# Performance work log

Measured on AMD Instinct MI355X. Metric: run time of the kernel, lower is better.

The kernel has to match this reference:

```python
import jax, jax.numpy as jnp
import numpy as np

# ---- static config (matches init_kwargs) ----
B, N_CAMS, C, H, W = 2, 6, 256, 32, 88
BEV_H = BEV_W = 100
NQ = BEV_H * BEV_W
D_PILLAR = 4
HEADS = 8
LEVELS = 3
HEAD_DIM = C // HEADS
PC_RANGE = (-51.2, -51.2, -5.0, 51.2, 51.2, 3.0)
OGFH, OGFW = 256, 704


def _make_lidar2img():
    """Plausible lidar->image projection matrices (K @ [R|t]) for 6 ring cameras."""
    mats = np.zeros((B, N_CAMS, 4, 4), np.float32)
    K = np.array([[557.0, 0.0, OGFW / 2.0], [0.0, 557.0, OGFH / 2.0], [0.0, 0.0, 1.0]], np.float64)
    for b in range(B):
        for n in range(N_CAMS):
            yaw = 2.0 * np.pi * n / N_CAMS + 0.05 * b
            fwd = np.array([np.cos(yaw), np.sin(yaw), 0.0])
            right = np.array([np.sin(yaw), -np.cos(yaw), 0.0])
            down = np.array([0.0, 0.0, -1.0])
            R = np.stack([right, down, fwd])  # lidar -> camera axes
            cam_center = np.array([1.5 * np.cos(yaw), 1.5 * np.sin(yaw), 1.8])
            t = -R @ cam_center
            P = K @ np.concatenate([R, t[:, None]], axis=1)
            mats[b, n, :3, :] = P.astype(np.float32)
            mats[b, n, 3, 3] = 1.0
    return jnp.asarray(mats)


def setup_inputs() -> dict:
    key = jax.random.key(0)
    ks = jax.random.split(key, 16)
    s = 0.02
    return {
        'imgs': jax.random.normal(ks[0], (B, N_CAMS, C, H, W), jnp.float32),
        'lidar2img': _make_lidar2img(),
        'bev_query': jax.random.normal(ks[1], (NQ, 1, C), jnp.float32) * s,
        'bev_pos': jax.random.normal(ks[2], (1, NQ, C), jnp.float32) * s,
        'cams_embeds': jax.random.normal(ks[3], (N_CAMS, C), jnp.float32) * s,
        'level_embeds': jax.random.normal(ks[4], (LEVELS, C), jnp.float32) * s,
        'w_fpn': jax.random.normal(ks[5], (LEVELS, C, C), jnp.float32) * s,
        'b_fpn': jnp.zeros((LEVELS, C), jnp.float32),
        'w_value': jax.random.normal(ks[6], (C, C), jnp.float32) * s,
        'b_value': jnp.zeros((C,), jnp.float32),
        'w_off': jax.random.normal(ks[7], (C, HEADS * LEVELS * D_PILLAR * 2), jnp.float32) * s,
        'b_off': jax.random.normal(ks[8], (HEADS * LEVELS * D_PILLAR * 2,), jnp.float32) * 0.5,
        'w_attn': jax.random.normal(ks[9], (C, HEADS * LEVELS * D_PILLAR), jnp.float32) * s,
        'b_attn': jnp.zeros((HEADS * LEVELS * D_PILLAR,), jnp.float32),
        'w_out': jax.random.normal(ks[10], (C, C), jnp.float32) * s,
        'b_out': jnp.zeros((C,), jnp.float32),
        'w_ts1': jax.random.normal(ks[11], (C, C), jnp.float32) * s,
        'b_ts1': jnp.zeros((C,), jnp.float32),
        'w_ts2': jax.random.normal(ks[12], (C, C), jnp.float32) * s,
        'b_ts2': jnp.zeros((C,), jnp.float32),
    }


def _deform_sample(v, loc, h, w):
    """Bilinear sample (grid_sample, zero padding, align_corners=False).
    v: [N, heads, h*w, dh]; loc: [N, heads, Q, 2] normalized to [0,1]. -> [N, heads, Q, dh]"""
    x = loc[..., 0] * w - 0.5
    y = loc[..., 1] * h - 0.5
    x0 = jnp.floor(x)
    y0 = jnp.floor(y)
    out = jnp.zeros(v.shape[:2] + (loc.shape[2], v.shape[-1]), v.dtype)
    for dx in (0, 1):
        for dy in (0, 1):
            xi = x0 + dx
            yi = y0 + dy
            wgt = (1.0 - jnp.abs(x - xi)) * (1.0 - jnp.abs(y - yi))
            valid = (xi >= 0) & (xi < w) & (yi >= 0) & (yi < h)
            idx = (jnp.clip(yi, 0, h - 1) * w + jnp.clip(xi, 0, w - 1)).astype(jnp.int32)
            g = jnp.take_along_axis(v, idx[..., None], axis=2)
            out = out + g * (wgt * valid)[..., None]
    return out


def _forward(imgs, lidar2img, bev_query, bev_pos, cams_embeds, level_embeds,
             w_fpn, b_fpn, w_value, b_value, w_off, b_off, w_attn, b_attn,
             w_out, b_out, w_ts1, b_ts1, w_ts2, b_ts2):
    # ---- FPN: 3 levels at strides 1/2/4 with per-level 1x1 projection ----
    x = imgs.reshape(B * N_CAMS, C, H, W)
    feats, shapes = [], []
    cur = x
    for l in range(LEVELS):
        if l > 0:
            bn, c, h, w = cur.shape
            cur = cur.reshape(bn, c, h // 2, 2, w // 2, 2).mean(axis=(3, 5))
        f = jnp.einsum('bchw,cd->bdhw', cur, w_fpn[l]) + b_fpn[l][None, :, None, None]
        feats.append(f)
        shapes.append((f.shape[2], f.shape[3]))
    # ---- flatten levels + cam/level embeds: [N, sum_hw, B, C] ----
    flat = []
    for l, f in enumerate(feats):
        h, w = shapes[l]
        fl = jnp.transpose(f.reshape(B, N_CAMS, C, h * w), (1, 0, 3, 2))  # [N,B,hw,C]
        fl = fl + cams_embeds[:, None, None, :] + level_embeds[l][None, None, None, :]
        flat.append(fl)
    feat_flatten = jnp.transpose(jnp.concatenate(flat, axis=2), (0, 2, 1, 3))  # [N,sum_hw,B,C]

    # ---- 3D pillar reference points, normalized [0,1] ----
    zrange = PC_RANGE[5] - PC_RANGE[2]
    zs = jnp.linspace(0.5, zrange - 0.5, D_PILLAR) / zrange
    xs = (jnp.arange(BEV_W, dtype=jnp.float32) + 0.5) / BEV_W
    ys = (jnp.arange(BEV_H, dtype=jnp.float32) + 0.5) / BEV_H
    gy, gx = jnp.meshgrid(ys, xs, indexing='ij')
    ref2d = jnp.stack([gx.ravel(), gy.ravel()], axis=-1)  # [NQ,2]
    ref3d = jnp.concatenate([
        jnp.broadcast_to(ref2d[None], (D_PILLAR, NQ, 2)),
        jnp.broadcast_to(zs[:, None, None].astype(jnp.float32), (D_PILLAR, NQ, 1)),
    ], axis=-1)
    scale = jnp.array([PC_RANGE[3] - PC_RANGE[0], PC_RANGE[4] - PC_RANGE[1], zrange], jnp.float32)
    shift = jnp.array(PC_RANGE[:3], jnp.float32)
    xyz = ref3d * scale + shift
    homog = jnp.concatenate([xyz, jnp.ones((D_PILLAR, NQ, 1), jnp.float32)], axis=-1)

    # ---- point sampling: project to each camera, mask invalid pixels ----
    pts = jnp.einsum('bnij,dqj->nbqdi', lidar2img, homog)  # [N,B,NQ,D,4]
    eps = 1e-5
    depth = pts[..., 2]
    xy = pts[..., :2] / jnp.maximum(depth[..., None], eps)
    ref_cam = xy / jnp.array([OGFW, OGFH], jnp.float32)  # [N,B,NQ,D,2]
    bev_mask = ((depth > eps) & (ref_cam[..., 0] > 0) & (ref_cam[..., 0] < 1)
                & (ref_cam[..., 1] > 0) & (ref_cam[..., 1] < 1))  # [N,B,NQ,D]

    pos = bev_pos[0]  # [NQ,C]

    def sca(query, value, ref_b, mask_b):
        # query [NQ,C]; value [N,sum_hw,C]; ref_b [N,NQ,D,2]; mask_b [N,NQ,D]
        residual = query
        q = query + pos
        v = value @ w_value + b_value
        off = (q @ w_off + b_off).reshape(NQ, HEADS, LEVELS, D_PILLAR, 2)
        attn = jax.nn.softmax((q @ w_attn + b_attn).reshape(NQ, HEADS, LEVELS * D_PILLAR), axis=-1)
        attn = attn.reshape(NQ, HEADS, LEVELS, D_PILLAR)
        out = jnp.zeros((N_CAMS, NQ, HEADS, HEAD_DIM), q.dtype)
        start = 0
        for l, (h, w) in enumerate(shapes):
            hw = h * w
            v_l = jnp.transpose(v[:, start:start + hw].reshape(N_CAMS, hw, HEADS, HEAD_DIM), (0, 2, 1, 3))
            start += hw
            norm = jnp.array([w, h], q.dtype)
            loc = ref_b[:, :, None, :, :] + off[None, :, :, l] / norm  # [N,NQ,heads,D,2]
            loc = jnp.transpose(loc, (0, 2, 1, 3, 4)).reshape(N_CAMS, HEADS, NQ * D_PILLAR, 2)
            s = _deform_sample(v_l, loc, h, w).reshape(N_CAMS, HEADS, NQ, D_PILLAR, HEAD_DIM)
            out = out + jnp.einsum('nhqpd,qhp->nqhd', s, attn[:, :, l])
        out = out.reshape(N_CAMS, NQ, C)
        valid = mask_b.any(axis=-1)  # [N,NQ]
        slots = (out * valid[..., None].astype(out.dtype)).sum(axis=0)
        count = jnp.maximum(valid.sum(axis=0), 1).astype(out.dtype)[:, None]
        slots = slots / count
        return slots @ w_out + b_out + residual

    def tsblock(t):
        return jax.nn.relu(t @ w_ts1 + b_ts1) @ w_ts2 + b_ts2

    bq = jnp.transpose(bev_query, (1, 0, 2))[0]  # [NQ,C]
    groups = []
    ego = bq
    for b in range(B):
        val = feat_flatten[:, :, b, :]
        r = ref_cam[:, b]
        m = bev_mask[:, b]
        if b == 0:
            for _ in range(2):
                bq = tsblock(sca(bq, val, r, m))
            ego = bq
            groups.append(ego.reshape(C, BEV_W, BEV_H))
        else:
            nb = tsblock(sca(ego, val, r, m))
            groups.append(nb.reshape(C, BEV_W, BEV_H))
    bev_groups = jnp.stack(groups, axis=0)  # [B,C,BEV_W,BEV_H]
    return bq[None], bev_groups


def reference(imgs, lidar2img, bev_query, bev_pos, cams_embeds, level_embeds,
              w_fpn, b_fpn, w_value, b_value, w_off, b_off, w_attn, b_attn,
              w_out, b_out, w_ts1, b_ts1, w_ts2, b_ts2):
    return _forward(imgs, lidar2img, bev_query, bev_pos, cams_embeds, level_embeds,
                    w_fpn, b_fpn, w_value, b_value, w_off, b_off, w_attn, b_attn,
                    w_out, b_out, w_ts1, b_ts1, w_ts2, b_ts2)
```

## Files before the change

kernel.cpp:

```cpp
#include <hip/hip_runtime.h>
#include <math.h>

typedef __attribute__((ext_vector_type(8))) short bf16x8;
typedef __attribute__((ext_vector_type(4))) float f32x4;

__device__ __forceinline__ unsigned short f2bf(float x) {
  union { float f; unsigned int u; } v; v.f = x;
  unsigned int r = v.u + 0x7fffu + ((v.u >> 16) & 1u);
  return (unsigned short)(r >> 16);
}
__device__ __forceinline__ float bf2f(unsigned short b) {
  union { unsigned int u; float f; } v; v.u = ((unsigned int)b) << 16; return v.f;
}
__device__ __forceinline__ void split2(float x, unsigned short& h, unsigned short& l) {
  h = f2bf(x);
  l = f2bf(x - bf2f(h));
}
__device__ __forceinline__ int fsi(int q, int c) { return q * 256 + (c ^ ((q & 7) << 2)); }

__device__ __forceinline__ void ld16(const unsigned short* b, bf16x8* f) {
  const unsigned short* b1 = b + 2048;
  const unsigned short* b2 = b + 4096;
  const unsigned short* b3 = b + 6144;
  asm volatile(
    "global_load_dwordx4 %0, %16, off\n\t"
    "global_load_dwordx4 %1, %16, off offset:1024\n\t"
    "global_load_dwordx4 %2, %16, off offset:2048\n\t"
    "global_load_dwordx4 %3, %16, off offset:3072\n\t"
    "global_load_dwordx4 %4, %17, off\n\t"
    "global_load_dwordx4 %5, %17, off offset:1024\n\t"
    "global_load_dwordx4 %6, %17, off offset:2048\n\t"
    "global_load_dwordx4 %7, %17, off offset:3072\n\t"
    "global_load_dwordx4 %8, %18, off\n\t"
    "global_load_dwordx4 %9, %18, off offset:1024\n\t"
    "global_load_dwordx4 %10, %18, off offset:2048\n\t"
    "global_load_dwordx4 %11, %18, off offset:3072\n\t"
    "global_load_dwordx4 %12, %19, off\n\t"
    "global_load_dwordx4 %13, %19, off offset:1024\n\t"
    "global_load_dwordx4 %14, %19, off offset:2048\n\t"
    "global_load_dwordx4 %15, %19, off offset:3072\n\t"
    "s_waitcnt vmcnt(0)"
    : "=&v"(f[0]), "=&v"(f[1]), "=&v"(f[2]), "=&v"(f[3]),
      "=&v"(f[4]), "=&v"(f[5]), "=&v"(f[6]), "=&v"(f[7]),
      "=&v"(f[8]), "=&v"(f[9]), "=&v"(f[10]), "=&v"(f[11]),
      "=&v"(f[12]), "=&v"(f[13]), "=&v"(f[14]), "=&v"(f[15])
    : "v"(b), "v"(b1), "v"(b2), "v"(b3));
}

#define MFMA(a, b, c) __builtin_amdgcn_mfma_f32_16x16x32_bf16(a, b, c, 0, 0, 0)

__device__ __forceinline__ void gemm2t32(
    const unsigned short* __restrict__ Wp, int tile0,
    int lane, int lk, int l15,
    const unsigned short (&AS)[2][32][32][8], f32x4 (&acc)[2][2])
{
  const unsigned short* base = Wp + ((size_t)(tile0 >> 1) * 16384) + (size_t)lane * 8;
  bf16x8 f[32];
  ld16(base, f);
  ld16(base + 8192, f + 16);
#pragma unroll
  for (int ks = 0; ks < 8; ++ks) {
    bf16x8 h0 = f[2 * ks], l0 = f[2 * ks + 1];
    bf16x8 h1 = f[16 + 2 * ks], l1 = f[17 + 2 * ks];
#pragma unroll
    for (int nf = 0; nf < 2; ++nf) {
      bf16x8 bqh = *(const bf16x8*)&AS[0][ks * 4 + lk][nf * 16 + l15][0];
      bf16x8 bql = *(const bf16x8*)&AS[1][ks * 4 + lk][nf * 16 + l15][0];
      acc[0][nf] = MFMA(h0, bqh, acc[0][nf]);
      acc[0][nf] = MFMA(h0, bql, acc[0][nf]);
      acc[0][nf] = MFMA(l0, bqh, acc[0][nf]);
      acc[1][nf] = MFMA(h1, bqh, acc[1][nf]);
      acc[1][nf] = MFMA(h1, bql, acc[1][nf]);
      acc[1][nf] = MFMA(l1, bqh, acc[1][nf]);
    }
  }
}

__device__ __forceinline__ void gemm2t64(
    const unsigned short* __restrict__ Wp, int tile0,
    int lane, int lk, int l15,
    const unsigned short (&AS)[2][32][64][8], f32x4 (&acc)[2][4])
{
  const unsigned short* base = Wp + ((size_t)(tile0 >> 1) * 16384) + (size_t)lane * 8;
  bf16x8 f[32];
  ld16(base, f);
  ld16(base + 8192, f + 16);
#pragma unroll
  for (int ks = 0; ks < 8; ++ks) {
    bf16x8 h0 = f[2 * ks], l0 = f[2 * ks + 1];
    bf16x8 h1 = f[16 + 2 * ks], l1 = f[17 + 2 * ks];
#pragma unroll
    for (int nf = 0; nf < 4; ++nf) {
      bf16x8 bqh = *(const bf16x8*)&AS[0][ks * 4 + lk][nf * 16 + l15][0];
      bf16x8 bql = *(const bf16x8*)&AS[1][ks * 4 + lk][nf * 16 + l15][0];
      acc[0][nf] = MFMA(h0, bqh, acc[0][nf]);
      acc[0][nf] = MFMA(h0, bql, acc[0][nf]);
      acc[0][nf] = MFMA(l0, bqh, acc[0][nf]);
      acc[1][nf] = MFMA(h1, bqh, acc[1][nf]);
      acc[1][nf] = MFMA(h1, bql, acc[1][nf]);
      acc[1][nf] = MFMA(l1, bqh, acc[1][nf]);
    }
  }
}

__device__ __forceinline__ void gemm1t64(
    const unsigned short* __restrict__ Wp, int tile,
    int lane, int lk, int l15,
    const unsigned short (&AS)[2][32][64][8], f32x4 (&acc)[4])
{
  const unsigned short* base = Wp + ((size_t)(tile >> 1) * 16384) + (size_t)(tile & 1) * 8192 + (size_t)lane * 8;
  bf16x8 f[16];
  ld16(base, f);
#pragma unroll
  for (int ks = 0; ks < 8; ++ks) {
    bf16x8 eh = f[2 * ks], el = f[2 * ks + 1];
#pragma unroll
    for (int nf = 0; nf < 4; ++nf) {
      bf16x8 bqh = *(const bf16x8*)&AS[0][ks * 4 + lk][nf * 16 + l15][0];
      bf16x8 bql = *(const bf16x8*)&AS[1][ks * 4 + lk][nf * 16 + l15][0];
      acc[nf] = MFMA(eh, bqh, acc[nf]);
      acc[nf] = MFMA(eh, bql, acc[nf]);
      acc[nf] = MFMA(el, bqh, acc[nf]);
    }
  }
}

__global__ __launch_bounds__(256) void pool2x2(const float* __restrict__ in, float* __restrict__ out,
                                               int h, int w, int total)
{
  int i = blockIdx.x * 256 + threadIdx.x;
  if (i >= total) return;
  int x = i % w; int r = i / w; int y = r % h; int ci = r / h;
  const float* p = in + (size_t)ci * (4 * h * w) + (size_t)(2 * y) * (2 * w) + 2 * x;
  out[i] = (p[0] + p[1] + p[2 * w] + p[2 * w + 1]) * 0.25f;
}

__global__ __launch_bounds__(256) void prep(
    const float* __restrict__ wo, const float* __restrict__ bo,
    const float* __restrict__ wa, const float* __restrict__ ba,
    const float* __restrict__ wout, const float* __restrict__ wts1, const float* __restrict__ wts2,
    const float* __restrict__ wfpn, const float* __restrict__ wval,
    const float* __restrict__ cams, const float* __restrict__ lev,
    const float* __restrict__ bfpn, const float* __restrict__ bval,
    unsigned short* __restrict__ wcatH, unsigned short* __restrict__ wcatL, float* __restrict__ bcat,
    unsigned short* __restrict__ woutH, unsigned short* __restrict__ woutL,
    unsigned short* __restrict__ wts1H, unsigned short* __restrict__ wts1L,
    unsigned short* __restrict__ w45H, unsigned short* __restrict__ w45L,
    unsigned short* __restrict__ wcombH, unsigned short* __restrict__ wcombL,
    float* __restrict__ e2)
{
  int bb = blockIdx.x, t = threadIdx.x;
  if (bb < 768) {
    int l = bb >> 8, i = bb & 255, j = t;
    const float* a = wfpn + ((size_t)l * 256 + i) * 256;
    float acc = 0.f;
    for (int k = 0; k < 256; ++k) acc = fmaf(a[k], wval[(size_t)k * 256 + j], acc);
    unsigned short h, lo; split2(acc, h, lo);
    size_t o = ((size_t)l * 256 + j) * 256 + i;
    wcombH[o] = h; wcombL[o] = lo;
  } else if (bb < 1056) {
    int i = (bb - 768) * 256 + t;
    int c = i >> 8, k = i & 255;
    float v = (c < 192) ? wo[k * 192 + c] : wa[k * 96 + (c - 192)];
    unsigned short h, l; split2(v, h, l);
    wcatH[i] = h; wcatL[i] = l;
    if (i < 288) bcat[i] = (i < 192) ? bo[i] : ba[i - 192];
  } else if (bb < 1312) {
    int i = (bb - 1056) * 256 + t;
    int nn = i >> 8, k = i & 255;
    float v = wout[(size_t)k * 256 + nn];
    unsigned short h, l; split2(v, h, l);
    woutH[i] = h; woutL[i] = l;
  } else if (bb < 1568) {
    int i = (bb - 1312) * 256 + t;
    int nn = i >> 8, k = i & 255;
    float v = wts1[(size_t)k * 256 + nn];
    unsigned short h, l; split2(v, h, l);
    wts1H[i] = h; wts1L[i] = l;
  } else if (bb < 1824) {
    int i = (bb - 1568) * 256 + t;
    int nn = i >> 8, k = i & 255;
    float v = wts2[(size_t)k * 256 + nn];
    unsigned short h, l; split2(v, h, l);
    w45H[i] = h; w45L[i] = l;
  } else if (bb < 2112) {
    int mp = bb - 1824;
    int k = t;
    float acc = 0.f;
    for (int j = 0; j < 256; ++j) {
      float wc = (mp < 192) ? wo[j * 192 + mp] : wa[j * 96 + (mp - 192)];
      acc = fmaf(wts2[(size_t)k * 256 + j], wc, acc);
    }
    unsigned short h, l; split2(acc, h, l);
    size_t o = (size_t)(256 + mp) * 256 + k;
    w45H[o] = h; w45L[o] = l;
  } else {
    int e = bb - 2112;
    int n = e / 3, l = e % 3, j = t;
    float acc = bval[j];
    for (int k = 0; k < 256; ++k) {
      float s = cams[n * 256 + k] + lev[l * 256 + k] + bfpn[l * 256 + k];
      acc = fmaf(s, wval[(size_t)k * 256 + j], acc);
    }
    e2[(size_t)e * 256 + j] = acc;
  }
}

__global__ __launch_bounds__(256) void relayout(
    const unsigned short* __restrict__ wcombH, const unsigned short* __restrict__ wcombL,
    const unsigned short* __restrict__ wcatH, const unsigned short* __restrict__ wcatL,
    const unsigned short* __restrict__ woutH, const unsigned short* __restrict__ woutL,
    const unsigned short* __restrict__ wts1H, const unsigned short* __restrict__ wts1L,
    const unsigned short* __restrict__ w45H, const unsigned short* __restrict__ w45L,
    unsigned short* __restrict__ wcombP, unsigned short* __restrict__ wcatP,
    unsigned short* __restrict__ woutP, unsigned short* __restrict__ wts1P,
    unsigned short* __restrict__ w45P)
{
  int bb = blockIdx.x, t = threadIdx.x;
  const unsigned short *H, *L; unsigned short* P; int tile;
  if (bb < 48)      { H = wcombH; L = wcombL; P = wcombP; tile = bb; }
  else if (bb < 66) { H = wcatH;  L = wcatL;  P = wcatP;  tile = bb - 48; }
  else if (bb < 82) { H = woutH;  L = woutL;  P = woutP;  tile = bb - 66; }
  else if (bb < 98) { H = wts1H;  L = wts1L;  P = wts1P;  tile = bb - 82; }
  else              { H = w45H;   L = w45L;   P = w45P;   tile = bb - 98; }
#pragma unroll
  for (int e = 0; e < 32; ++e) {
    int idx = t * 32 + e;
    int slot = idx >> 9;
    int lane = (idx >> 3) & 63;
    int j8 = idx & 7;
    int ks = slot >> 1, hl = slot & 1;
    int col = tile * 16 + (lane & 15);
    int k = ks * 32 + (lane >> 4) * 8 + j8;
    size_t dst = ((size_t)(tile >> 1) * 16384) + (size_t)(((tile & 1) << 4) + slot) * 512 + (size_t)lane * 8 + j8;
    P[dst] = (hl ? L : H)[(size_t)col * 256 + k];
  }
}

__global__ __launch_bounds__(512) void value_fused(
    const float* __restrict__ img0, const float* __restrict__ cur1, const float* __restrict__ cur2,
    const unsigned short* __restrict__ wcombP,
    const float* __restrict__ e2, float* __restrict__ V)
{
  __shared__ __align__(16) unsigned short AS[2][32][32][8];
  int t = threadIdx.x, wid = t >> 6, lane = t & 63, l15 = lane & 15, lk = lane >> 4;
  int bx = blockIdx.x, cam = blockIdx.y;
  int level, tb, hw; const float* src;
  if (bx < 88)       { level = 0; tb = bx;       hw = 2816; src = img0; }
  else if (bx < 110) { level = 1; tb = bx - 88;  hw = 704;  src = cur1; }
  else               { level = 2; tb = bx - 110; hw = 176;  src = cur2; }
  int p0 = tb * 32;
  const int LST[3] = {0, 2816, 3520};
  src += (size_t)cam * 256 * hw;

  {
    int f4g = t & 7, kb = t >> 3;
    bool full = (p0 + 32 <= hw);
#pragma unroll
    for (int j = 0; j < 4; ++j) {
      int k = kb + j * 64;
      const float* row = src + (size_t)k * hw;
      int p = p0 + 4 * f4g;
      float4 v;
      if (full) v = *(const float4*)(row + p);
      else {
        v.x = (p < hw) ? row[p] : 0.f;     v.y = (p + 1 < hw) ? row[p + 1] : 0.f;
        v.z = (p + 2 < hw) ? row[p + 2] : 0.f; v.w = (p + 3 < hw) ? row[p + 3] : 0.f;
      }
      int ch = k >> 3, ko = k & 7;
      unsigned short h, l;
      split2(v.x, h, l); AS[0][ch][4 * f4g + 0][ko] = h; AS[1][ch][4 * f4g + 0][ko] = l;
      split2(v.y, h, l); AS[0][ch][4 * f4g + 1][ko] = h; AS[1][ch][4 * f4g + 1][ko] = l;
      split2(v.z, h, l); AS[0][ch][4 * f4g + 2][ko] = h; AS[1][ch][4 * f4g + 2][ko] = l;
      split2(v.w, h, l); AS[0][ch][4 * f4g + 3][ko] = h; AS[1][ch][4 * f4g + 3][ko] = l;
    }
  }
  __syncthreads();

  f32x4 zed = {0.f, 0.f, 0.f, 0.f};
  f32x4 acc[2][2] = {{zed, zed}, {zed, zed}};
  gemm2t32(wcombP, level * 16 + wid * 2, lane, lk, l15, AS, acc);
  __syncthreads();

  float* ASf = (float*)(&AS[0][0][0][0]);
  const float* bias = e2 + (size_t)(cam * 3 + level) * 256;
#pragma unroll
  for (int mf = 0; mf < 2; ++mf) {
    int chb = (wid * 2 + mf) * 16 + lk * 4;
    float4 b4 = *(const float4*)(bias + chb);
#pragma unroll
    for (int nf = 0; nf < 2; ++nf) {
      int q = nf * 16 + l15;
      float4 o;
      o.x = acc[mf][nf][0] + b4.x; o.y = acc[mf][nf][1] + b4.y;
      o.z = acc[mf][nf][2] + b4.z; o.w = acc[mf][nf][3] + b4.w;
      *(float4*)&ASf[fsi(q, chb)] = o;
    }
  }
  __syncthreads();
  float* Vb = V + ((size_t)cam * 3696 + LST[level] + p0) * 256;
#pragma unroll
  for (int j = 0; j < 4; ++j) {
    int g = t + j * 512;
    int q = g >> 6, c = (g & 63) * 4;
    if (p0 + q < hw)
      *(float4*)(Vb + (size_t)q * 256 + c) = *(const float4*)&ASf[fsi(q, c)];
  }
}

__global__ __launch_bounds__(512) void fused_iter(
    const float* __restrict__ slots, const float* __restrict__ qin,
    const float* __restrict__ pos2, const float* __restrict__ rowbias,
    const unsigned short* __restrict__ woutP, const unsigned short* __restrict__ wts1P,
    const unsigned short* __restrict__ w45P, const unsigned short* __restrict__ wcatP,
    const float* __restrict__ bout, const float* __restrict__ bts1,
    const float* __restrict__ bts2, const float* __restrict__ bcat,
    float* __restrict__ qout, float* __restrict__ outA, float* __restrict__ outB,
    float* __restrict__ qtmpA, float* __restrict__ qtmpB, int init)
{
  __shared__ __align__(16) unsigned short AS[2][32][64][8];
  float* ASf = (float*)(&AS[0][0][0][0]);
  int t = threadIdx.x, wid = t >> 6, lane = t & 63, l15 = lane & 15, lk = lane >> 4;
  int r0 = blockIdx.x * 64;
  f32x4 zed = {0.f, 0.f, 0.f, 0.f};

  {
    const float* base = init ? qin : slots;
#pragma unroll
    for (int j = 0; j < 8; ++j) {
      int g = t + j * 512;
      int q = g >> 6, c = (g & 63) * 4;
      int rq = r0 + q; if (rq > 9999) rq = 9999;
      float4 a = *(const float4*)(base + (size_t)rq * 256 + c);
      if (init) {
        if (pos2) {
          float4 p = *(const float4*)(pos2 + (size_t)rq * 256 + c);
          a.x += p.x; a.y += p.y; a.z += p.z; a.w += p.w;
        }
        if (rowbias) {
          float4 rb = *(const float4*)(rowbias + c);
          a.x += rb.x; a.y += rb.y; a.z += rb.z; a.w += rb.w;
        }
      }
      ushort4 hh, ll;
      split2(a.x, hh.x, ll.x); split2(a.y, hh.y, ll.y);
      split2(a.z, hh.z, ll.z); split2(a.w, hh.w, ll.w);
      *(ushort4*)&AS[0][c >> 3][q][c & 7] = hh;
      *(ushort4*)&AS[1][c >> 3][q][c & 7] = ll;
    }
  }
  __syncthreads();

  if (init) {
    f32x4 acc[2][4] = {{zed, zed, zed, zed}, {zed, zed, zed, zed}};
    gemm2t64(wcatP, wid * 2, lane, lk, l15, AS, acc);
    f32x4 acc3[4] = {zed, zed, zed, zed};
    if (wid < 2) gemm1t64(wcatP, 16 + wid, lane, lk, l15, AS, acc3);
    __syncthreads();
#pragma unroll
    for (int mf = 0; mf < 2; ++mf) {
      int chb = (wid * 2 + mf) * 16 + lk * 4;
      float4 b4 = *(const float4*)(bcat + chb);
#pragma unroll
      for (int nf = 0; nf < 4; ++nf) {
        int q = nf * 16 + l15;
        float4 o;
        o.x = acc[mf][nf][0] + b4.x; o.y = acc[mf][nf][1] + b4.y;
        o.z = acc[mf][nf][2] + b4.z; o.w = acc[mf][nf][3] + b4.w;
        *(float4*)&ASf[fsi(q, chb)] = o;
      }
    }
    if (wid < 2) {
      int ce = wid * 16 + lk * 4;
      float4 b4 = *(const float4*)(bcat + 256 + ce);
#pragma unroll
      for (int nf = 0; nf < 4; ++nf) {
        int qg = r0 + nf * 16 + l15;
        if (qg < 10000) {
          float4 o;
          o.x = acc3[nf][0] + b4.x; o.y = acc3[nf][1] + b4.y;
          o.z = acc3[nf][2] + b4.z; o.w = acc3[nf][3] + b4.w;
          *(float4*)(qtmpB + (size_t)qg * 32 + ce) = o;
        }
      }
    }
    __syncthreads();
#pragma unroll
    for (int j = 0; j < 8; ++j) {
      int g = t + j * 512;
      int q = g >> 6, c = (g & 63) * 4;
      int qg = r0 + q;
      if (qg < 10000)
        *(float4*)(qtmpA + (size_t)qg * 256 + c) = *(const float4*)&ASf[fsi(q, c)];
    }
    return;
  }

  {
    f32x4 acc[2][4] = {{zed, zed, zed, zed}, {zed, zed, zed, zed}};
    gemm2t64(woutP, wid * 2, lane, lk, l15, AS, acc);
    __syncthreads();
    float4 qreg[8];
#pragma unroll
    for (int j = 0; j < 8; ++j) {
      int g = t + j * 512;
      int q = g >> 6, c = (g & 63) * 4;
      int rq = r0 + q; if (rq > 9999) rq = 9999;
      qreg[j] = *(const float4*)(qin + (size_t)rq * 256 + c);
    }
#pragma unroll
    for (int j = 0; j < 8; ++j) {
      int g = t + j * 512;
      int q = g >> 6, c = (g & 63) * 4;
      *(float4*)&ASf[fsi(q, c)] = qreg[j];
    }
    __syncthreads();
    float4 rr[2][4];
#pragma unroll
    for (int mf = 0; mf < 2; ++mf) {
      int chb = (wid * 2 + mf) * 16 + lk * 4;
#pragma unroll
      for (int nf = 0; nf < 4; ++nf)
        rr[mf][nf] = *(const float4*)&ASf[fsi(nf * 16 + l15, chb)];
    }
    __syncthreads();
#pragma unroll
    for (int mf = 0; mf < 2; ++mf) {
      int chb = (wid * 2 + mf) * 16 + lk * 4;
      float4 b4 = *(const float4*)(bout + chb);
#pragma unroll
      for (int nf = 0; nf < 4; ++nf) {
        int q = nf * 16 + l15;
        float v0 = acc[mf][nf][0] + b4.x + rr[mf][nf].x;
        float v1 = acc[mf][nf][1] + b4.y + rr[mf][nf].y;
        float v2 = acc[mf][nf][2] + b4.z + rr[mf][nf].z;
        float v3 = acc[mf][nf][3] + b4.w + rr[mf][nf].w;
        ushort4 hh, ll;
        split2(v0, hh.x, ll.x); split2(v1, hh.y, ll.y);
        split2(v2, hh.z, ll.z); split2(v3, hh.w, ll.w);
        *(ushort4*)&AS[0][chb >> 3][q][chb & 7] = hh;
        *(ushort4*)&AS[1][chb >> 3][q][chb & 7] = ll;
      }
    }
    __syncthreads();
  }
  {
    f32x4 acc[2][4] = {{zed, zed, zed, zed}, {zed, zed, zed, zed}};
    gemm2t64(wts1P, wid * 2, lane, lk, l15, AS, acc);
    __syncthreads();
#pragma unroll
    for (int mf = 0; mf < 2; ++mf) {
      int chb = (wid * 2 + mf) * 16 + lk * 4;
      float4 b4 = *(const float4*)(bts1 + chb);
#pragma unroll
      for (int nf = 0; nf < 4; ++nf) {
        int q = nf * 16 + l15;
        float v0 = fmaxf(acc[mf][nf][0] + b4.x, 0.f);
        float v1 = fmaxf(acc[mf][nf][1] + b4.y, 0.f);
        float v2 = fmaxf(acc[mf][nf][2] + b4.z, 0.f);
        float v3 = fmaxf(acc[mf][nf][3] + b4.w, 0.f);
        ushort4 hh, ll;
        split2(v0, hh.x, ll.x); split2(v1, hh.y, ll.y);
        split2(v2, hh.z, ll.z); split2(v3, hh.w, ll.w);
        *(ushort4*)&AS[0][chb >> 3][q][chb & 7] = hh;
        *(ushort4*)&AS[1][chb >> 3][q][chb & 7] = ll;
      }
    }
    __syncthreads();
  }
  {
    f32x4 accA[2][4] = {{zed, zed, zed, zed}, {zed, zed, zed, zed}};
    f32x4 accB[2][4] = {{zed, zed, zed, zed}, {zed, zed, zed, zed}};
    if (wid < 4 || qtmpA) {
      gemm2t64(w45P, wid * 4,     lane, lk, l15, AS, accA);
      gemm2t64(w45P, wid * 4 + 2, lane, lk, l15, AS, accB);
    }
    f32x4 acc3[4] = {zed, zed, zed, zed};
    if (qtmpA && wid < 2) gemm1t64(w45P, 32 + wid, lane, lk, l15, AS, acc3);
    __syncthreads();
    if (wid < 4) {
#pragma unroll
      for (int half = 0; half < 2; ++half) {
#pragma unroll
        for (int mf = 0; mf < 2; ++mf) {
          int chb = (wid * 4 + half * 2 + mf) * 16 + lk * 4;
          float4 b4 = *(const float4*)(bts2 + chb);
#pragma unroll
          for (int nf = 0; nf < 4; ++nf) {
            int q = nf * 16 + l15;
            f32x4 a = half ? accB[mf][nf] : accA[mf][nf];
            float4 o;
            o.x = a[0] + b4.x; o.y = a[1] + b4.y;
            o.z = a[2] + b4.z; o.w = a[3] + b4.w;
            *(float4*)&ASf[fsi(q, chb)] = o;
          }
        }
      }
    }
    if (qtmpA && wid < 2) {
      int ce = wid * 16 + lk * 4;
#pragma unroll
      for (int nf = 0; nf < 4; ++nf) {
        int qg = r0 + nf * 16 + l15;
        if (qg < 10000) {
          float4 o;
          o.x = acc3[nf][0]; o.y = acc3[nf][1]; o.z = acc3[nf][2]; o.w = acc3[nf][3];
          *(float4*)(qtmpB + (size_t)qg * 32 + ce) = o;
        }
      }
    }
    __syncthreads();
#pragma unroll
    for (int j = 0; j < 8; ++j) {
      int g = t + j * 512;
      int q = g >> 6, c = (g & 63) * 4;
      int qg = r0 + q;
      if (qg < 10000) {
        float4 vq = *(const float4*)&ASf[fsi(q, c)];
        size_t go = (size_t)qg * 256 + c;
        *(float4*)(qout + go) = vq;
        if (outA) { *(float4*)(outA + go) = vq; *(float4*)(outB + go) = vq; }
      }
    }
    if (!qtmpA) return;
    __syncthreads();
    if (wid >= 4) {
#pragma unroll
      for (int half = 0; half < 2; ++half) {
#pragma unroll
        for (int mf = 0; mf < 2; ++mf) {
          int cc = ((wid - 4) * 4 + half * 2 + mf) * 16 + lk * 4;
#pragma unroll
          for (int nf = 0; nf < 4; ++nf) {
            int q = nf * 16 + l15;
            f32x4 a = half ? accB[mf][nf] : accA[mf][nf];
            float4 o;
            o.x = a[0]; o.y = a[1]; o.z = a[2]; o.w = a[3];
            *(float4*)&ASf[fsi(q, cc)] = o;
          }
        }
      }
    }
    __syncthreads();
#pragma unroll
    for (int j = 0; j < 8; ++j) {
      int g = t + j * 512;
      int q = g >> 6, c = (g & 63) * 4;
      int qg = r0 + q;
      if (qg < 10000)
        *(float4*)(qtmpA + (size_t)qg * 256 + c) = *(const float4*)&ASf[fsi(q, c)];
    }
  }
}

__global__ __launch_bounds__(256) void sca_sample(const float* __restrict__ qtmpA, const float* __restrict__ qtmpB,
                                                  const float* __restrict__ posA, const float* __restrict__ posB,
                                                  const float* __restrict__ V,
                                                  const float* __restrict__ l2i, float* __restrict__ slots)
{
  int b = blockIdx.x;
  int q = (b & 7) * 1250 + (b >> 3);
  int t = threadIdx.x;
  int head = t >> 5;
  __shared__ float raw[288];
  __shared__ float attnS[96];
  __shared__ float refx[6][4], refy[6][4];
  __shared__ int mnd[24];
  __shared__ int validn[6];
  __shared__ __align__(16) float w4[576][4];
  __shared__ __align__(16) int o4[576][4];

  {
    float x = qtmpA[(size_t)q * 256 + t];
    if (posA) x += posA[(size_t)q * 256 + t];
    raw[t] = x;
    if (t < 32) {
      float y = qtmpB[(size_t)q * 32 + t];
      if (posB) y += posB[(size_t)q * 32 + t];
      raw[256 + t] = y;
    }
  }
  if (t >= 32 && t < 56) {
    int tt = t - 32;
    int n = tt >> 2, d = tt & 3;
    const float* Mrow = l2i + n * 16;
    int qx = q % 100, qy = q / 100;
    float X = ((qx + 0.5f) / 100.0f) * 102.4f + (-51.2f);
    float Y = ((qy + 0.5f) / 100.0f) * 102.4f + (-51.2f);
    float zi = (d == 3) ? 7.5f : (0.5f + (float)d * (7.0f / 3.0f));
    float Z = zi + (-5.0f);
    float px = Mrow[0] * X + Mrow[1] * Y + Mrow[2] * Z + Mrow[3];
    float py = Mrow[4] * X + Mrow[5] * Y + Mrow[6] * Z + Mrow[7];
    float pz = Mrow[8] * X + Mrow[9] * Y + Mrow[10] * Z + Mrow[11];
    float dz = fmaxf(pz, 1e-5f);
    float xc = (px / dz) / 704.0f;
    float yc = (py / dz) / 256.0f;
    refx[n][d] = xc; refy[n][d] = yc;
    mnd[n * 4 + d] = (pz > 1e-5f) && (xc > 0.f) && (xc < 1.f) && (yc > 0.f) && (yc < 1.f);
  }
  __syncthreads();
  if (t < 8) {
    float mx = raw[192 + t * 12];
    for (int p = 1; p < 12; ++p) mx = fmaxf(mx, raw[192 + t * 12 + p]);
    float s = 0.f;
    float e[12];
#pragma unroll
    for (int p = 0; p < 12; ++p) { e[p] = __expf(raw[192 + t * 12 + p] - mx); s += e[p]; }
    float inv = 1.f / s;
#pragma unroll
    for (int p = 0; p < 12; ++p) attnS[t * 12 + p] = e[p] * inv;
  } else if (t < 14) {
    int n = t - 8;
    validn[n] = mnd[n * 4] | mnd[n * 4 + 1] | mnd[n * 4 + 2] | mnd[n * 4 + 3];
  }
  __syncthreads();

  int nv = validn[0] + validn[1] + validn[2] + validn[3] + validn[4] + validn[5];
  float invc = 1.f / (float)(nv > 1 ? nv : 1);

  const float WWf[3] = {88.f, 44.f, 22.f}, HHf[3] = {32.f, 16.f, 8.f};
  const int WWi[3] = {88, 44, 22}, STi[3] = {0, 2816, 3520};
  for (int pt = t; pt < 576; pt += 256) {
    int hd = pt & 7;
    int g = pt >> 3;
    int j = g % 12, n = g / 12;
    int l = j >> 2, d = j & 3;
    float wwf = WWf[l], hhf = HHf[l];
    int wwi = WWi[l], st = STi[l];
    float a = attnS[hd * 12 + j] * invc;
    float ox = raw[hd * 24 + l * 8 + d * 2 + 0];
    float oy = raw[hd * 24 + l * 8 + d * 2 + 1];
    float x = refx[n][d] * wwf + ox - 0.5f;
    float y = refy[n][d] * hhf + oy - 0.5f;
    float x0 = floorf(x), y0 = floorf(y);
    float fx = x - x0, fy = y - y0;
    float wx0 = 1.f - fx, wy0 = 1.f - fy;
    float vx0 = (x0 >= 0.f && x0 < wwf) ? 1.f : 0.f;
    float vx1 = (x0 + 1.f >= 0.f && x0 + 1.f < wwf) ? 1.f : 0.f;
    float vy0 = (y0 >= 0.f && y0 < hhf) ? 1.f : 0.f;
    float vy1 = (y0 + 1.f >= 0.f && y0 + 1.f < hhf) ? 1.f : 0.f;
    w4[pt][0] = a * wx0 * wy0 * vx0 * vy0;
    w4[pt][1] = a * fx * wy0 * vx1 * vy0;
    w4[pt][2] = a * wx0 * fy * vx0 * vy1;
    w4[pt][3] = a * fx * fy * vx1 * vy1;
    int ix0 = (int)fminf(fmaxf(x0, 0.f), wwf - 1.f);
    int ix1 = (int)fminf(fmaxf(x0 + 1.f, 0.f), wwf - 1.f);
    int iy0 = (int)fminf(fmaxf(y0, 0.f), hhf - 1.f);
    int iy1 = (int)fminf(fmaxf(y0 + 1.f, 0.f), hhf - 1.f);
    int rA = (st + iy0 * wwi) * 256, rB = (st + iy1 * wwi) * 256;
    o4[pt][0] = rA + ix0 * 256;
    o4[pt][1] = rA + ix1 * 256;
    o4[pt][2] = rB + ix0 * 256;
    o4[pt][3] = rB + ix1 * 256;
  }
  __syncthreads();

  float acc0 = 0.f, acc1 = 0.f;
#pragma unroll
  for (int n = 0; n < 6; ++n) {
    if (!validn[n]) continue;
    const float* Vn = V + (size_t)n * 946176 + t;
    int pb = n * 96 + head;
    float va[48];
#pragma unroll
    for (int j = 0; j < 12; ++j) {
      int4 o = *reinterpret_cast<const int4*>(&o4[pb + j * 8][0]);
      va[4 * j + 0] = Vn[o.x];
      va[4 * j + 1] = Vn[o.y];
      va[4 * j + 2] = Vn[o.z];
      va[4 * j + 3] = Vn[o.w];
    }
#pragma unroll
    for (int j = 0; j < 12; ++j) {
      float4 w = *reinterpret_cast<const float4*>(&w4[pb + j * 8][0]);
      acc0 = fmaf(w.x, va[4 * j + 0], acc0);
      acc1 = fmaf(w.y, va[4 * j + 1], acc1);
      acc0 = fmaf(w.z, va[4 * j + 2], acc0);
      acc1 = fmaf(w.w, va[4 * j + 3], acc1);
    }
  }
  slots[(size_t)q * 256 + t] = acc0 + acc1;
}

extern "C" void kernel_launch(void* const* d_in, const int* in_sizes, int n_in,
                              void* d_out, int out_size, void* d_ws, size_t ws_size,
                              hipStream_t stream)
{
  const float* imgs = (const float*)d_in[0];
  const float* l2i = (const float*)d_in[1];
  const float* bev_query = (const float*)d_in[2];
  const float* bev_pos = (const float*)d_in[3];
  const float* cams = (const float*)d_in[4];
  const float* lev = (const float*)d_in[5];
  const float* wfpn = (const float*)d_in[6];
  const float* bfpn = (const float*)d_in[7];
  const float* wval = (const float*)d_in[8];
  const float* bval = (const float*)d_in[9];
  const float* woff = (const float*)d_in[10];
  const float* boff = (const float*)d_in[11];
  const float* wattn = (const float*)d_in[12];
  const float* battn = (const float*)d_in[13];
  const float* wout = (const float*)d_in[14];
  const float* bout = (const float*)d_in[15];
  const float* wts1 = (const float*)d_in[16];
  const float* bts1 = (const float*)d_in[17];
  const float* wts2 = (const float*)d_in[18];
  const float* bts2 = (const float*)d_in[19];

  float* W = (float*)d_ws;
  size_t off = 0;
  auto alloc = [&](size_t n) { float* p = W + off; off += n; return p; };
  float* v    = alloc((size_t)6 * 3696 * 256);
  float* cur1 = alloc((size_t)12 * 256 * 16 * 44);
  float* cur2 = alloc((size_t)12 * 256 * 8 * 22);
  float* bqA  = alloc(2560000);
  float* bqB  = alloc(2560000);
  float* qtmpA = alloc(2560000);
  float* qtmpB = alloc(320000);
  float* posA = alloc(2560000);
  float* posB = alloc(320000);
  float* slots = alloc(2560000);
  float* wcatR = alloc(73728);
  float* woutR = alloc(65536);
  float* wts1R = alloc(65536);
  float* w45R = alloc(139264);
  float* wcombR = alloc(196608);
  float* wcombPR = alloc(196608);
  float* wcatPR = alloc(73728);
  float* woutPR = alloc(65536);
  float* wts1PR = alloc(65536);
  float* w45PR = alloc(139264);
  float* bcat = alloc(512);
  float* e2 = alloc(4608);
  (void)ws_size; (void)in_sizes; (void)n_in; (void)out_size;

  unsigned short* wcat_h = (unsigned short*)wcatR;   unsigned short* wcat_l = wcat_h + 288 * 256;
  unsigned short* wout_h = (unsigned short*)woutR;   unsigned short* wout_l = wout_h + 65536;
  unsigned short* wts1_h = (unsigned short*)wts1R;   unsigned short* wts1_l = wts1_h + 65536;
  unsigned short* w45_h = (unsigned short*)w45R;     unsigned short* w45_l = w45_h + 544 * 256;
  unsigned short* wcomb_h = (unsigned short*)wcombR; unsigned short* wcomb_l = wcomb_h + 3 * 65536;
  unsigned short* wcombP = (unsigned short*)wcombPR;
  unsigned short* wcatP = (unsigned short*)wcatPR;
  unsigned short* woutP = (unsigned short*)woutPR;
  unsigned short* wts1P = (unsigned short*)wts1PR;
  unsigned short* w45P = (unsigned short*)w45PR;

  float* OUT = (float*)d_out;

  pool2x2<<<8448, 256, 0, stream>>>(imgs, cur1, 16, 44, 2162688);
  pool2x2<<<2112, 256, 0, stream>>>(cur1, cur2, 8, 22, 540672);
  prep<<<2130, 256, 0, stream>>>(woff, boff, wattn, battn, wout, wts1, wts2, wfpn, wval,
                                 cams, lev, bfpn, bval,
                                 wcat_h, wcat_l, bcat, wout_h, wout_l, wts1_h, wts1_l,
                                 w45_h, w45_l, wcomb_h, wcomb_l, e2);
  relayout<<<132, 256, 0, stream>>>(wcomb_h, wcomb_l, wcat_h, wcat_l, wout_h, wout_l,
                                    wts1_h, wts1_l, w45_h, w45_l,
                                    wcombP, wcatP, woutP, wts1P, w45P);

  fused_iter<<<157, 512, 0, stream>>>(nullptr, bev_pos, nullptr, bts2,
      woutP, wts1P, w45P, wcatP, bout, bts1, bts2, bcat,
      nullptr, nullptr, nullptr, posA, posB, 1);
  fused_iter<<<157, 512, 0, stream>>>(nullptr, bev_query, bev_pos, nullptr,
      woutP, wts1P, w45P, wcatP, bout, bts1, bts2, bcat,
      nullptr, nullptr, nullptr, qtmpA, qtmpB, 1);

  value_fused<<<dim3(116, 6), 512, 0, stream>>>(imgs, cur1, cur2, wcombP, e2, v);

  sca_sample<<<10000, 256, 0, stream>>>(qtmpA, qtmpB, nullptr, nullptr, v, l2i, slots);
  fused_iter<<<157, 512, 0, stream>>>(slots, bev_query, nullptr, nullptr,
      woutP, wts1P, w45P, wcatP, bout, bts1, bts2, bcat,
      bqA, nullptr, nullptr, qtmpA, qtmpB, 0);
  sca_sample<<<10000, 256, 0, stream>>>(qtmpA, qtmpB, posA, posB, v, l2i, slots);
  fused_iter<<<157, 512, 0, stream>>>(slots, bqA, nullptr, nullptr,
      woutP, wts1P, w45P, wcatP, bout, bts1, bts2, bcat,
      bqB, OUT, OUT + 2560000, qtmpA, qtmpB, 0);

  value_fused<<<dim3(116, 6), 512, 0, stream>>>(imgs + (size_t)4325376, cur1 + (size_t)1081344,
                                                cur2 + (size_t)270336, wcombP, e2, v);
  sca_sample<<<10000, 256, 0, stream>>>(qtmpA, qtmpB, posA, posB, v, l2i + 96, slots);
  fused_iter<<<157, 512, 0, stream>>>(slots, bqB, nullptr, nullptr,
      woutP, wts1P, w45P, wcatP, bout, bts1, bts2, bcat,
      OUT + 5120000, nullptr, nullptr, nullptr, nullptr, 0);
}
```

Before: 320.7 us.

## Halve fused_iter row tile to 32 and compact valid-camera sampling points

```diff
diff --git a/kernel.cpp b/kernel.cpp
--- a/kernel.cpp
+++ b/kernel.cpp
@@ -76,37 +76,10 @@
   }
 }
 
-__device__ __forceinline__ void gemm2t64(
-    const unsigned short* __restrict__ Wp, int tile0,
-    int lane, int lk, int l15,
-    const unsigned short (&AS)[2][32][64][8], f32x4 (&acc)[2][4])
-{
-  const unsigned short* base = Wp + ((size_t)(tile0 >> 1) * 16384) + (size_t)lane * 8;
-  bf16x8 f[32];
-  ld16(base, f);
-  ld16(base + 8192, f + 16);
-#pragma unroll
-  for (int ks = 0; ks < 8; ++ks) {
-    bf16x8 h0 = f[2 * ks], l0 = f[2 * ks + 1];
-    bf16x8 h1 = f[16 + 2 * ks], l1 = f[17 + 2 * ks];
-#pragma unroll
-    for (int nf = 0; nf < 4; ++nf) {
-      bf16x8 bqh = *(const bf16x8*)&AS[0][ks * 4 + lk][nf * 16 + l15][0];
-      bf16x8 bql = *(const bf16x8*)&AS[1][ks * 4 + lk][nf * 16 + l15][0];
-      acc[0][nf] = MFMA(h0, bqh, acc[0][nf]);
-      acc[0][nf] = MFMA(h0, bql, acc[0][nf]);
-      acc[0][nf] = MFMA(l0, bqh, acc[0][nf]);
-      acc[1][nf] = MFMA(h1, bqh, acc[1][nf]);
-      acc[1][nf] = MFMA(h1, bql, acc[1][nf]);
-      acc[1][nf] = MFMA(l1, bqh, acc[1][nf]);
-    }
-  }
-}
-
-__device__ __forceinline__ void gemm1t64(
+__device__ __forceinline__ void gemm1t32(
     const unsigned short* __restrict__ Wp, int tile,
     int lane, int lk, int l15,
-    const unsigned short (&AS)[2][32][64][8], f32x4 (&acc)[4])
+    const unsigned short (&AS)[2][32][32][8], f32x4 (&acc)[2])
 {
   const unsigned short* base = Wp + ((size_t)(tile >> 1) * 16384) + (size_t)(tile & 1) * 8192 + (size_t)lane * 8;
   bf16x8 f[16];
@@ -115,7 +88,7 @@
   for (int ks = 0; ks < 8; ++ks) {
     bf16x8 eh = f[2 * ks], el = f[2 * ks + 1];
 #pragma unroll
-    for (int nf = 0; nf < 4; ++nf) {
+    for (int nf = 0; nf < 2; ++nf) {
       bf16x8 bqh = *(const bf16x8*)&AS[0][ks * 4 + lk][nf * 16 + l15][0];
       bf16x8 bql = *(const bf16x8*)&AS[1][ks * 4 + lk][nf * 16 + l15][0];
       acc[nf] = MFMA(eh, bqh, acc[nf]);
@@ -237,7 +210,7 @@
   }
 }
 
-__global__ __launch_bounds__(512) void value_fused(
+__global__ __launch_bounds__(512, 4) void value_fused(
     const float* __restrict__ img0, const float* __restrict__ cur1, const float* __restrict__ cur2,
     const unsigned short* __restrict__ wcombP,
     const float* __restrict__ e2, float* __restrict__ V)
@@ -308,7 +281,7 @@
   }
 }
 
-__global__ __launch_bounds__(512) void fused_iter(
+__global__ __launch_bounds__(512, 4) void fused_iter(
     const float* __restrict__ slots, const float* __restrict__ qin,
     const float* __restrict__ pos2, const float* __restrict__ rowbias,
     const unsigned short* __restrict__ woutP, const unsigned short* __restrict__ wts1P,
@@ -318,16 +291,16 @@
     float* __restrict__ qout, float* __restrict__ outA, float* __restrict__ outB,
     float* __restrict__ qtmpA, float* __restrict__ qtmpB, int init)
 {
-  __shared__ __align__(16) unsigned short AS[2][32][64][8];
+  __shared__ __align__(16) unsigned short AS[2][32][32][8];
   float* ASf = (float*)(&AS[0][0][0][0]);
   int t = threadIdx.x, wid = t >> 6, lane = t & 63, l15 = lane & 15, lk = lane >> 4;
-  int r0 = blockIdx.x * 64;
+  int r0 = blockIdx.x * 32;
   f32x4 zed = {0.f, 0.f, 0.f, 0.f};
 
   {
     const float* base = init ? qin : slots;
 #pragma unroll
-    for (int j = 0; j < 8; ++j) {
+    for (int j = 0; j < 4; ++j) {
       int g = t + j * 512;
       int q = g >> 6, c = (g & 63) * 4;
       int rq = r0 + q; if (rq > 9999) rq = 9999;
@@ -352,17 +325,17 @@
   __syncthreads();
 
   if (init) {
-    f32x4 acc[2][4] = {{zed, zed, zed, zed}, {zed, zed, zed, zed}};
-    gemm2t64(wcatP, wid * 2, lane, lk, l15, AS, acc);
-    f32x4 acc3[4] = {zed, zed, zed, zed};
-    if (wid < 2) gemm1t64(wcatP, 16 + wid, lane, lk, l15, AS, acc3);
+    f32x4 acc[2][2] = {{zed, zed}, {zed, zed}};
+    gemm2t32(wcatP, wid * 2, lane, lk, l15, AS, acc);
+    f32x4 acc3[2] = {zed, zed};
+    if (wid < 2) gemm1t32(wcatP, 16 + wid, lane, lk, l15, AS, acc3);
     __syncthreads();
 #pragma unroll
     for (int mf = 0; mf < 2; ++mf) {
       int chb = (wid * 2 + mf) * 16 + lk * 4;
       float4 b4 = *(const float4*)(bcat + chb);
 #pragma unroll
-      for (int nf = 0; nf < 4; ++nf) {
+      for (int nf = 0; nf < 2; ++nf) {
         int q = nf * 16 + l15;
         float4 o;
         o.x = acc[mf][nf][0] + b4.x; o.y = acc[mf][nf][1] + b4.y;
@@ -374,7 +347,7 @@
       int ce = wid * 16 + lk * 4;
       float4 b4 = *(const float4*)(bcat + 256 + ce);
 #pragma unroll
-      for (int nf = 0; nf < 4; ++nf) {
+      for (int nf = 0; nf < 2; ++nf) {
         int qg = r0 + nf * 16 + l15;
         if (qg < 10000) {
           float4 o;
@@ -386,7 +359,7 @@
     }
     __syncthreads();
 #pragma unroll
-    for (int j = 0; j < 8; ++j) {
+    for (int j = 0; j < 4; ++j) {
       int g = t + j * 512;
       int q = g >> 6, c = (g & 63) * 4;
       int qg = r0 + q;
@@ -397,30 +370,30 @@
   }
 
   {
-    f32x4 acc[2][4] = {{zed, zed, zed, zed}, {zed, zed, zed, zed}};
-    gemm2t64(woutP, wid * 2, lane, lk, l15, AS, acc);
-    __syncthreads();
-    float4 qreg[8];
-#pragma unroll
-    for (int j = 0; j < 8; ++j) {
+    f32x4 acc[2][2] = {{zed, zed}, {zed, zed}};
+    gemm2t32(woutP, wid * 2, lane, lk, l15, AS, acc);
+    __syncthreads();
+    float4 qreg[4];
+#pragma unroll
+    for (int j = 0; j < 4; ++j) {
       int g = t + j * 512;
       int q = g >> 6, c = (g & 63) * 4;
       int rq = r0 + q; if (rq > 9999) rq = 9999;
       qreg[j] = *(const float4*)(qin + (size_t)rq * 256 + c);
     }
 #pragma unroll
-    for (int j = 0; j < 8; ++j) {
+    for (int j = 0; j < 4; ++j) {
       int g = t + j * 512;
       int q = g >> 6, c = (g & 63) * 4;
       *(float4*)&ASf[fsi(q, c)] = qreg[j];
     }
     __syncthreads();
-    float4 rr[2][4];
+    float4 rr[2][2];
 #pragma unroll
     for (int mf = 0; mf < 2; ++mf) {
       int chb = (wid * 2 + mf) * 16 + lk * 4;
 #pragma unroll
-      for (int nf = 0; nf < 4; ++nf)
+      for (int nf = 0; nf < 2; ++nf)
         rr[mf][nf] = *(const float4*)&ASf[fsi(nf * 16 + l15, chb)];
     }
     __syncthreads();
@@ -429,7 +402,7 @@
       int chb = (wid * 2 + mf) * 16 + lk * 4;
       float4 b4 = *(const float4*)(bout + chb);
 #pragma unroll
-      for (int nf = 0; nf < 4; ++nf) {
+      for (int nf = 0; nf < 2; ++nf) {
         int q = nf * 16 + l15;
         float v0 = acc[mf][nf][0] + b4.x + rr[mf][nf].x;
         float v1 = acc[mf][nf][1] + b4.y + rr[mf][nf].y;
@@ -445,15 +418,15 @@
     __syncthreads();
   }
   {
-    f32x4 acc[2][4] = {{zed, zed, zed, zed}, {zed, zed, zed, zed}};
-    gemm2t64(wts1P, wid * 2, lane, lk, l15, AS, acc);
+    f32x4 acc[2][2] = {{zed, zed}, {zed, zed}};
+    gemm2t32(wts1P, wid * 2, lane, lk, l15, AS, acc);
     __syncthreads();
 #pragma unroll
     for (int mf = 0; mf < 2; ++mf) {
       int chb = (wid * 2 + mf) * 16 + lk * 4;
       float4 b4 = *(const float4*)(bts1 + chb);
 #pragma unroll
-      for (int nf = 0; nf < 4; ++nf) {
+      for (int nf = 0; nf < 2; ++nf) {
         int q = nf * 16 + l15;
         float v0 = fmaxf(acc[mf][nf][0] + b4.x, 0.f);
         float v1 = fmaxf(acc[mf][nf][1] + b4.y, 0.f);
@@ -469,14 +442,14 @@
     __syncthreads();
   }
   {
-    f32x4 accA[2][4] = {{zed, zed, zed, zed}, {zed, zed, zed, zed}};
-    f32x4 accB[2][4] = {{zed, zed, zed, zed}, {zed, zed, zed, zed}};
+    f32x4 accA[2][2] = {{zed, zed}, {zed, zed}};
+    f32x4 accB[2][2] = {{zed, zed}, {zed, zed}};
     if (wid < 4 || qtmpA) {
-      gemm2t64(w45P, wid * 4,     lane, lk, l15, AS, accA);
-      gemm2t64(w45P, wid * 4 + 2, lane, lk, l15, AS, accB);
-    }
-    f32x4 acc3[4] = {zed, zed, zed, zed};
-    if (qtmpA && wid < 2) gemm1t64(w45P, 32 + wid, lane, lk, l15, AS, acc3);
+      gemm2t32(w45P, wid * 4,     lane, lk, l15, AS, accA);
+      gemm2t32(w45P, wid * 4 + 2, lane, lk, l15, AS, accB);
+    }
+    f32x4 acc3[2] = {zed, zed};
+    if (qtmpA && wid < 2) gemm1t32(w45P, 32 + wid, lane, lk, l15, AS, acc3);
     __syncthreads();
     if (wid < 4) {
 #pragma unroll
@@ -486,7 +459,7 @@
           int chb = (wid * 4 + half * 2 + mf) * 16 + lk * 4;
           float4 b4 = *(const float4*)(bts2 + chb);
 #pragma unroll
-          for (int nf = 0; nf < 4; ++nf) {
+          for (int nf = 0; nf < 2; ++nf) {
             int q = nf * 16 + l15;
             f32x4 a = half ? accB[mf][nf] : accA[mf][nf];
             float4 o;
@@ -500,7 +473,7 @@
     if (qtmpA && wid < 2) {
       int ce = wid * 16 + lk * 4;
 #pragma unroll
-      for (int nf = 0; nf < 4; ++nf) {
+      for (int nf = 0; nf < 2; ++nf) {
         int qg = r0 + nf * 16 + l15;
         if (qg < 10000) {
           float4 o;
@@ -511,7 +484,7 @@
     }
     __syncthreads();
 #pragma unroll
-    for (int j = 0; j < 8; ++j) {
+    for (int j = 0; j < 4; ++j) {
       int g = t + j * 512;
       int q = g >> 6, c = (g & 63) * 4;
       int qg = r0 + q;
@@ -531,7 +504,7 @@
         for (int mf = 0; mf < 2; ++mf) {
           int cc = ((wid - 4) * 4 + half * 2 + mf) * 16 + lk * 4;
 #pragma unroll
-          for (int nf = 0; nf < 4; ++nf) {
+          for (int nf = 0; nf < 2; ++nf) {
             int q = nf * 16 + l15;
             f32x4 a = half ? accB[mf][nf] : accA[mf][nf];
             float4 o;
@@ -543,7 +516,7 @@
     }
     __syncthreads();
 #pragma unroll
-    for (int j = 0; j < 8; ++j) {
+    for (int j = 0; j < 4; ++j) {
       int g = t + j * 512;
       int q = g >> 6, c = (g & 63) * 4;
       int qg = r0 + q;
@@ -615,15 +588,20 @@
   }
   __syncthreads();
 
-  int nv = validn[0] + validn[1] + validn[2] + validn[3] + validn[4] + validn[5];
+  int packed = 0, nv = 0;
+#pragma unroll
+  for (int n = 0; n < 6; ++n)
+    if (validn[n]) { packed |= n << (3 * nv); nv++; }
   float invc = 1.f / (float)(nv > 1 ? nv : 1);
 
   const float WWf[3] = {88.f, 44.f, 22.f}, HHf[3] = {32.f, 16.f, 8.f};
   const int WWi[3] = {88, 44, 22}, STi[3] = {0, 2816, 3520};
-  for (int pt = t; pt < 576; pt += 256) {
+  int npts = nv * 96;
+  for (int pt = t; pt < npts; pt += 256) {
     int hd = pt & 7;
     int g = pt >> 3;
-    int j = g % 12, n = g / 12;
+    int j = g % 12, ni = g / 12;
+    int n = (packed >> (3 * ni)) & 7;
     int l = j >> 2, d = j & 3;
     float wwf = WWf[l], hhf = HHf[l];
     int wwi = WWi[l], st = STi[l];
@@ -647,28 +625,31 @@
     int ix1 = (int)fminf(fmaxf(x0 + 1.f, 0.f), wwf - 1.f);
     int iy0 = (int)fminf(fmaxf(y0, 0.f), hhf - 1.f);
     int iy1 = (int)fminf(fmaxf(y0 + 1.f, 0.f), hhf - 1.f);
-    int rA = (st + iy0 * wwi) * 256, rB = (st + iy1 * wwi) * 256;
-    o4[pt][0] = rA + ix0 * 256;
-    o4[pt][1] = rA + ix1 * 256;
-    o4[pt][2] = rB + ix0 * 256;
-    o4[pt][3] = rB + ix1 * 256;
+    int rA = (st + iy0 * wwi) << 10, rB = (st + iy1 * wwi) << 10;
+    o4[pt][0] = rA + (ix0 << 10);
+    o4[pt][1] = rA + (ix1 << 10);
+    o4[pt][2] = rB + (ix0 << 10);
+    o4[pt][3] = rB + (ix1 << 10);
   }
   __syncthreads();
 
+  int t4 = t << 2;
   float acc0 = 0.f, acc1 = 0.f;
+  int sl = 0;
 #pragma unroll
   for (int n = 0; n < 6; ++n) {
     if (!validn[n]) continue;
-    const float* Vn = V + (size_t)n * 946176 + t;
-    int pb = n * 96 + head;
+    const char* Vn = (const char*)(V + (size_t)n * 946176);
+    int pb = sl * 96 + head;
+    sl++;
     float va[48];
 #pragma unroll
     for (int j = 0; j < 12; ++j) {
       int4 o = *reinterpret_cast<const int4*>(&o4[pb + j * 8][0]);
-      va[4 * j + 0] = Vn[o.x];
-      va[4 * j + 1] = Vn[o.y];
-      va[4 * j + 2] = Vn[o.z];
-      va[4 * j + 3] = Vn[o.w];
+      va[4 * j + 0] = *(const float*)(Vn + (unsigned)(o.x + t4));
+      va[4 * j + 1] = *(const float*)(Vn + (unsigned)(o.y + t4));
+      va[4 * j + 2] = *(const float*)(Vn + (unsigned)(o.z + t4));
+      va[4 * j + 3] = *(const float*)(Vn + (unsigned)(o.w + t4));
     }
 #pragma unroll
     for (int j = 0; j < 12; ++j) {
@@ -757,28 +738,28 @@
                                     wts1_h, wts1_l, w45_h, w45_l,
                                     wcombP, wcatP, woutP, wts1P, w45P);
 
-  fused_iter<<<157, 512, 0, stream>>>(nullptr, bev_pos, nullptr, bts2,
+  fused_iter<<<313, 512, 0, stream>>>(nullptr, bev_pos, nullptr, bts2,
       woutP, wts1P, w45P, wcatP, bout, bts1, bts2, bcat,
       nullptr, nullptr, nullptr, posA, posB, 1);
-  fused_iter<<<157, 512, 0, stream>>>(nullptr, bev_query, bev_pos, nullptr,
+  fused_iter<<<313, 512, 0, stream>>>(nullptr, bev_query, bev_pos, nullptr,
       woutP, wts1P, w45P, wcatP, bout, bts1, bts2, bcat,
       nullptr, nullptr, nullptr, qtmpA, qtmpB, 1);
 
   value_fused<<<dim3(116, 6), 512, 0, stream>>>(imgs, cur1, cur2, wcombP, e2, v);
 
   sca_sample<<<10000, 256, 0, stream>>>(qtmpA, qtmpB, nullptr, nullptr, v, l2i, slots);
-  fused_iter<<<157, 512, 0, stream>>>(slots, bev_query, nullptr, nullptr,
+  fused_iter<<<313, 512, 0, stream>>>(slots, bev_query, nullptr, nullptr,
       woutP, wts1P, w45P, wcatP, bout, bts1, bts2, bcat,
       bqA, nullptr, nullptr, qtmpA, qtmpB, 0);
   sca_sample<<<10000, 256, 0, stream>>>(qtmpA, qtmpB, posA, posB, v, l2i, slots);
-  fused_iter<<<157, 512, 0, stream>>>(slots, bqA, nullptr, nullptr,
+  fused_iter<<<313, 512, 0, stream>>>(slots, bqA, nullptr, nullptr,
       woutP, wts1P, w45P, wcatP, bout, bts1, bts2, bcat,
       bqB, OUT, OUT + 2560000, qtmpA, qtmpB, 0);
 
   value_fused<<<dim3(116, 6), 512, 0, stream>>>(imgs + (size_t)4325376, cur1 + (size_t)1081344,
                                                 cur2 + (size_t)270336, wcombP, e2, v);
   sca_sample<<<10000, 256, 0, stream>>>(qtmpA, qtmpB, posA, posB, v, l2i + 96, slots);
-  fused_iter<<<157, 512, 0, stream>>>(slots, bqB, nullptr, nullptr,
+  fused_iter<<<313, 512, 0, stream>>>(slots, bqB, nullptr, nullptr,
       woutP, wts1P, w45P, wcatP, bout, bts1, bts2, bcat,
       OUT + 5120000, nullptr, nullptr, nullptr, nullptr, 0);
 }
```

After: 444.7 us. 38.7% more time.
